# Kernel optimization log

Measured on AMD Instinct MI355X. Metric: run time of the kernel, lower is better.

Reference implementation:

```python
import jax, jax.numpy as jnp
import numpy as np

E, D, A, F, K = 512, 1024, 128, 32, 31  # encoder_dim, decoder_dim, attention_dim, location_filters, kernel
B, T = 128, 512


def setup_inputs() -> dict:
    key = jax.random.key(0)
    ks = jax.random.split(key, 9)
    s = lambda *sh: 1.0 / np.sqrt(sh[-1])
    return {
        "encoder_outputs": jax.random.normal(ks[0], (B, T, E), jnp.float32),
        "decoder_state": jax.random.normal(ks[1], (B, D), jnp.float32),
        "prev_attention_weights": jax.random.uniform(ks[2], (B, T), jnp.float32),
        # parameters (torch Linear stores [out, in]; Conv1d [out, in, K])
        "W_enc": jax.random.normal(ks[3], (A, E), jnp.float32) * s(A, E),
        "W_dec": jax.random.normal(ks[4], (A, D), jnp.float32) * s(A, D),
        "conv_w": jax.random.normal(ks[5], (F, 1, K), jnp.float32) * (1.0 / np.sqrt(K)),
        "W_loc": jax.random.normal(ks[6], (A, F), jnp.float32) * s(A, F),
        "W_e": jax.random.normal(ks[7], (1, A), jnp.float32) * s(1, A),
        "b_e": jax.random.normal(ks[8], (1,), jnp.float32) * 0.01,
    }


def reference(encoder_outputs, decoder_state, prev_attention_weights,
              W_enc, W_dec, conv_w, W_loc, W_e, b_e):
    # encoder projection: [B,T,E] @ [E,A] -> [B,T,A]
    enc_p = jnp.einsum('bte,ae->bta', encoder_outputs, W_enc)
    # decoder projection: [B,D] -> [B,1,A]
    dec_p = jnp.einsum('bd,ad->ba', decoder_state, W_dec)[:, None, :]
    # location conv: [B,1,T] * [F,1,K] -> [B,F,T], 'same' padding
    loc = jax.lax.conv_general_dilated(
        prev_attention_weights[:, None, :], conv_w,
        window_strides=(1,), padding=[((K - 1) // 2, (K - 1) // 2)],
        dimension_numbers=('NCH', 'OIH', 'NCH'))
    # [B,F,T] -> [B,T,A]
    loc_p = jnp.einsum('bft,af->bta', loc, W_loc)
    # energies: [B,T]
    energies = jnp.einsum('bta,a->bt', jnp.tanh(enc_p + dec_p + loc_p), W_e[0]) + b_e[0]
    attention_weights = jax.nn.softmax(energies, axis=1)
    # context: [B,T] x [B,T,E] -> [B,E]
    context_vector = jnp.einsum('bt,bte->be', attention_weights, encoder_outputs)
    return context_vector, attention_weights
```

## Files before the change

### kernel.cpp

```cpp
#include <hip/hip_runtime.h>
#include <hip/hip_bf16.h>
#include <math.h>

namespace {
constexpr int EDIM  = 512;
constexpr int DDIM  = 1024;
constexpr int ADIM  = 128;
constexpr int FDIM  = 32;
constexpr int KW    = 31;
constexpr int BATCH = 128;
constexpr int TDIM  = 512;

constexpr int LSTR = 40;
constexpr int TILE = 128 * LSTR;

typedef __attribute__((ext_vector_type(8))) short short8;
typedef __attribute__((ext_vector_type(4))) float floatx4;

__device__ __forceinline__ float fast_tanh(float x) {
  x = fminf(9.0f, fmaxf(-9.0f, x));
  float e = __expf(2.0f * x);
  return (e - 1.0f) / (e + 1.0f);
}

__device__ __forceinline__ ushort2 pack_bf16(float x, float y) {
  union { __hip_bfloat162 h; ushort2 u; } cv;
  cv.h = __float22bfloat162_rn(make_float2(x, y));
  return cv.u;
}

__device__ __forceinline__ short8 pack8(floatx4 a, floatx4 b) {
  union { ushort2 u[4]; short8 v; } o;
  o.u[0] = pack_bf16(a[0], a[1]); o.u[1] = pack_bf16(a[2], a[3]);
  o.u[2] = pack_bf16(b[0], b[1]); o.u[3] = pack_bf16(b[2], b[3]);
  return o.v;
}

__device__ __forceinline__ int ld_acq(int* p) {
  return __hip_atomic_load(p, __ATOMIC_ACQUIRE, __HIP_MEMORY_SCOPE_WORKGROUP);
}
__device__ __forceinline__ void add_rel(int* p) {
  __hip_atomic_fetch_add(p, 1, __ATOMIC_RELEASE, __HIP_MEMORY_SCOPE_WORKGROUP);
}

__global__ __launch_bounds__(256)
void dec_proj_kernel(const float* __restrict__ dec,
                     const float* __restrict__ Wdec,
                     float* __restrict__ dec_p) {
  int b = blockIdx.x, az = blockIdx.y;
  int tid = threadIdx.x;
  int al = tid >> 3, seg = tid & 7;
  int a = az * 32 + al;
  const float* dv = dec + (size_t)b * DDIM;
  const float* wv = Wdec + (size_t)a * DDIM;
  float s = 0.f;
  #pragma unroll 8
  for (int it = 0; it < 32; ++it) {
    int d = it * 32 + seg * 4;
    float4 d4 = *(const float4*)(dv + d);
    float4 w4 = *(const float4*)(wv + d);
    s += d4.x * w4.x + d4.y * w4.y + d4.z * w4.z + d4.w * w4.w;
  }
  s += __shfl_xor(s, 1, 64);
  s += __shfl_xor(s, 2, 64);
  s += __shfl_xor(s, 4, 64);
  if (seg == 0) dec_p[b * ADIM + a] = s;
}

template <int FUSED>
__global__ __launch_bounds__(768)
void energies_kernel(const float* __restrict__ enc,
                     const float* __restrict__ Wenc,
                     const float* __restrict__ pa,
                     const float* __restrict__ convw,
                     const float* __restrict__ Wloc,
                     const float* __restrict__ We,
                     const float* __restrict__ be,
                     const float* __restrict__ dec_p_g,
                     const float* __restrict__ dec,
                     const float* __restrict__ Wdec,
                     float* __restrict__ energ,
                     float* __restrict__ pm,
                     float* __restrict__ ps,
                     float* __restrict__ pctx) {
  __shared__ ushort tiles[2 * 2 * TILE];
  __shared__ ushort convS[4096];
  __shared__ float pa_s[160];
  __shared__ float cw_t[KW * 32];
  __shared__ int ready_a[2], ready_b[2], done_c[2], conv_done, dp_done;
  __shared__ float e_s[128];
  __shared__ float aw_s[128];
  __shared__ float ms[2];
  __shared__ float red2[6][512];
  __shared__ float dps[ADIM];

  const int tid  = threadIdx.x;
  const int b    = blockIdx.y;
  const int chunk = blockIdx.x;
  const int t0b  = chunk * 128;
  const int wave = tid >> 6, lane = tid & 63;

  if (tid == 0) {
    ready_a[0] = ready_a[1] = ready_b[0] = ready_b[1] = 0;
    done_c[0] = done_c[1] = 0;
    conv_done = 0;
    dp_done = 0;
  }
  if (tid >= 512 && tid < 512 + 158) {
    int gt = t0b - 15 + (tid - 512);
    pa_s[tid - 512] = (gt >= 0 && gt < TDIM) ? pa[b * TDIM + gt] : 0.f;
  }
  if (tid < 512)
    for (int id = tid; id < FDIM * KW; id += 512)
      cw_t[(id % KW) * 32 + (id / KW)] = convw[id];
  __syncthreads();

  if (wave >= 8) {
    const bool isA = (wave < 10);
    const int p = wave & 1;
    const float* gbase = isA ? enc + ((size_t)(b * TDIM + t0b)) * EDIM : Wenc;
    ushort* lbase = tiles + (isA ? 0 : TILE);
    int* myready = isA ? ready_a : ready_b;

    floatx4 v[8];
    #pragma unroll
    for (int j = 0; j < 4; ++j) {
      int idx = j * 64 + lane;
      int row = p * 64 + (idx >> 2), c = idx & 3;
      const float* g = gbase + (size_t)row * EDIM + c * 8;
      v[2 * j]     = *(const floatx4*)g;
      v[2 * j + 1] = *(const floatx4*)(g + 4);
    }

    for (int kt = 0; kt < 16; ++kt) {
      const int s = kt & 1, i = kt >> 1;
      if (kt >= 2)
        while (ld_acq(&done_c[s]) < 8 * i) __builtin_amdgcn_s_sleep(10);
      ushort* slot = lbase + s * 2 * TILE;
      #pragma unroll
      for (int j = 0; j < 4; ++j) {
        int idx = j * 64 + lane;
        int row = p * 64 + (idx >> 2), c = idx & 3;
        *(short8*)&slot[row * LSTR + c * 8] = pack8(v[2 * j], v[2 * j + 1]);
      }
      __threadfence_block();
      if (lane == 0) add_rel(&myready[s]);
      if (kt < 15) {
        #pragma unroll
        for (int j = 0; j < 4; ++j) {
          int idx = j * 64 + lane;
          int row = p * 64 + (idx >> 2), c = idx & 3;
          const float* g = gbase + (size_t)row * EDIM + (kt + 1) * 32 + c * 8;
          v[2 * j]     = *(const floatx4*)g;
          v[2 * j + 1] = *(const floatx4*)(g + 4);
        }
      }
    }

    if constexpr (!FUSED) return;

    {
      const int pidx = (wave - 8) * 64 + lane;
      const int a = pidx >> 1, half = pidx & 1;
      const float* dv = dec + (size_t)b * DDIM + half * 512;
      const float* wv = Wdec + (size_t)a * DDIM + half * 512;
      float s = 0.f;
      #pragma unroll 8
      for (int it = 0; it < 128; ++it) {
        floatx4 d4 = *(const floatx4*)(dv + it * 4);
        floatx4 w4 = *(const floatx4*)(wv + it * 4);
        s += d4[0] * w4[0] + d4[1] * w4[1] + d4[2] * w4[2] + d4[3] * w4[3];
      }
      s += __shfl_xor(s, 1, 64);
      if (half == 0) dps[a] = s;
      __threadfence_block();
      if (lane == 0) add_rel(&dp_done);
    }
  } else {
    const int lc = lane & 15, lq = lane >> 4;

    {
      const int tl = tid >> 2, fg = tid & 3;
      float cv[8] = {0.f, 0.f, 0.f, 0.f, 0.f, 0.f, 0.f, 0.f};
      #pragma unroll
      for (int k = 0; k < KW; ++k) {
        float p = pa_s[tl + k];
        floatx4 c0 = *(const floatx4*)&cw_t[k * 32 + fg * 8];
        floatx4 c1 = *(const floatx4*)&cw_t[k * 32 + fg * 8 + 4];
        #pragma unroll
        for (int n = 0; n < 4; ++n) cv[n] += p * c0[n];
        #pragma unroll
        for (int n = 0; n < 4; ++n) cv[4 + n] += p * c1[n];
      }
      *(short8*)&convS[tl * 32 + fg * 8] =
          pack8((floatx4){cv[0], cv[1], cv[2], cv[3]},
                (floatx4){cv[4], cv[5], cv[6], cv[7]});
    }
    __threadfence_block();
    if (lane == 0) add_rel(&conv_done);

    floatx4 acc[8];
    #pragma unroll
    for (int aT = 0; aT < 8; ++aT) acc[aT] = (floatx4){0.f, 0.f, 0.f, 0.f};

    for (int kt = 0; kt < 16; ++kt) {
      const int s = kt & 1, i = kt >> 1;
      const int need = 2 * (i + 1);
      while (ld_acq(&ready_a[s]) < need || ld_acq(&ready_b[s]) < need)
        __builtin_amdgcn_s_sleep(6);
      const ushort* As_ = tiles + s * 2 * TILE;
      const ushort* Bs_ = As_ + TILE;
      short8 af = *(const short8*)&As_[(wave * 16 + lc) * LSTR + lq * 8];
      #pragma unroll
      for (int aT = 0; aT < 8; ++aT) {
        short8 bf = *(const short8*)&Bs_[(aT * 16 + lc) * LSTR + lq * 8];
        acc[aT] = __builtin_amdgcn_mfma_f32_16x16x32_bf16(af, bf, acc[aT], 0, 0, 0);
      }
      if (lane == 0) add_rel(&done_c[s]);
    }

    while (ld_acq(&conv_done) < 8) __builtin_amdgcn_s_sleep(6);
    {
      short8 afl = *(const short8*)&convS[(wave * 16 + lc) * 32 + lq * 8];
      #pragma unroll
      for (int aT = 0; aT < 8; ++aT) {
        const float* g = Wloc + (size_t)(aT * 16 + lc) * FDIM + lq * 8;
        short8 bfl = pack8(*(const floatx4*)g, *(const floatx4*)(g + 4));
        acc[aT] = __builtin_amdgcn_mfma_f32_16x16x32_bf16(afl, bfl, acc[aT], 0, 0, 0);
      }
    }

    const float be0 = be[0];
    float dpv[8], wev[8];
    if constexpr (FUSED) {
      while (ld_acq(&dp_done) < 4) __builtin_amdgcn_s_sleep(6);
    }
    #pragma unroll
    for (int aT = 0; aT < 8; ++aT) {
      int a = aT * 16 + lc;
      dpv[aT] = FUSED ? dps[a] : dec_p_g[b * ADIM + a];
      wev[aT] = We[a];
    }
    {
      float es[4] = {0.f, 0.f, 0.f, 0.f};
      #pragma unroll
      for (int aT = 0; aT < 8; ++aT)
        #pragma unroll
        for (int i = 0; i < 4; ++i)
          es[i] += fast_tanh(acc[aT][i] + dpv[aT]) * wev[aT];
      #pragma unroll
      for (int m = 1; m < 16; m <<= 1)
        #pragma unroll
        for (int i = 0; i < 4; ++i) es[i] += __shfl_xor(es[i], m, 64);
      if (lc == 0) {
        floatx4 ev = {es[0] + be0, es[1] + be0, es[2] + be0, es[3] + be0};
        *(floatx4*)&energ[(size_t)b * TDIM + t0b + wave * 16 + lq * 4] = ev;
        if (FUSED) *(floatx4*)&e_s[wave * 16 + lq * 4] = ev;
      }
    }
  }

  if constexpr (!FUSED) return;

  __syncthreads();

  if (wave == 0) {
    float x0 = e_s[lane], x1 = e_s[lane + 64];
    float m = fmaxf(x0, x1);
    #pragma unroll
    for (int off = 1; off < 64; off <<= 1) m = fmaxf(m, __shfl_xor(m, off, 64));
    float sum = __expf(x0 - m) + __expf(x1 - m);
    #pragma unroll
    for (int off = 1; off < 64; off <<= 1) sum += __shfl_xor(sum, off, 64);
    if (lane == 0) {
      ms[0] = m;
      pm[b * 4 + chunk] = m;
      ps[b * 4 + chunk] = sum;
    }
  }
  __syncthreads();
  const float mI = ms[0];
  if (tid < 128) aw_s[tid] = __expf(e_s[tid] - mI);
  __syncthreads();

  {
    const int tg = tid >> 7;
    const int c4 = (tid & 127) * 4;
    const float* ep = enc + ((size_t)(b * TDIM + t0b)) * EDIM + c4;
    float4 acc = make_float4(0.f, 0.f, 0.f, 0.f);
    for (int t = tg; t < 128; t += 6) {
      float w = aw_s[t];
      float4 v = *(const float4*)(ep + (size_t)t * EDIM);
      acc.x += w * v.x; acc.y += w * v.y; acc.z += w * v.z; acc.w += w * v.w;
    }
    *(float4*)&red2[tg][c4] = acc;
  }
  __syncthreads();
  if (tid < 512) {
    float v = 0.f;
    #pragma unroll
    for (int g = 0; g < 6; ++g) v += red2[g][tid];
    pctx[((size_t)(b * 4 + chunk)) * EDIM + tid] = v;
  }
}

__global__ __launch_bounds__(512)
void combine_kernel(const float* __restrict__ energ,
                    const float* __restrict__ pm,
                    const float* __restrict__ ps,
                    const float* __restrict__ pctx,
                    float* __restrict__ attn,
                    float* __restrict__ ctx) {
  const int b = blockIdx.x, tid = threadIdx.x;
  const float m0 = pm[b * 4 + 0], m1 = pm[b * 4 + 1];
  const float m2 = pm[b * 4 + 2], m3 = pm[b * 4 + 3];
  const float M = fmaxf(fmaxf(m0, m1), fmaxf(m2, m3));
  const float r0 = __expf(m0 - M), r1 = __expf(m1 - M);
  const float r2 = __expf(m2 - M), r3 = __expf(m3 - M);
  const float S = ps[b * 4 + 0] * r0 + ps[b * 4 + 1] * r1 +
                  ps[b * 4 + 2] * r2 + ps[b * 4 + 3] * r3;
  const float inv = 1.0f / S;
  const float e = energ[(size_t)b * TDIM + tid];
  attn[(size_t)b * TDIM + tid] = __expf(e - M) * inv;
  const float* pc = pctx + (size_t)b * 4 * EDIM + tid;
  const float c = pc[0] * r0 + pc[EDIM] * r1 + pc[2 * EDIM] * r2 +
                  pc[3 * EDIM] * r3;
  ctx[(size_t)b * EDIM + tid] = c * inv;
}

__global__ __launch_bounds__(256)
void softmax_context_inplace_kernel(const float* __restrict__ enc,
                                    float* __restrict__ attn,
                                    float* __restrict__ ctx) {
  __shared__ float aw[TDIM];
  __shared__ float redm[4];
  __shared__ float reds[4];
  const int b = blockIdx.y, tid = threadIdx.x;
  float* row = attn + (size_t)b * TDIM;
  float x0 = row[tid], x1 = row[tid + 256];
  float m = fmaxf(x0, x1);
  #pragma unroll
  for (int off = 32; off; off >>= 1) m = fmaxf(m, __shfl_xor(m, off, 64));
  int wid = tid >> 6, lane = tid & 63;
  if (lane == 0) redm[wid] = m;
  __syncthreads();
  m = fmaxf(fmaxf(redm[0], redm[1]), fmaxf(redm[2], redm[3]));
  float e0 = __expf(x0 - m), e1 = __expf(x1 - m);
  float s = e0 + e1;
  #pragma unroll
  for (int off = 32; off; off >>= 1) s += __shfl_xor(s, off, 64);
  if (lane == 0) reds[wid] = s;
  __syncthreads();
  s = reds[0] + reds[1] + reds[2] + reds[3];
  float inv = 1.0f / s;
  float w0 = e0 * inv, w1 = e1 * inv;
  row[tid] = w0; row[tid + 256] = w1;
  aw[tid] = w0; aw[tid + 256] = w1;
  __syncthreads();
  const float* ep = enc + ((size_t)b * TDIM) * EDIM;
  float a0 = 0.f, a1 = 0.f;
  #pragma unroll 8
  for (int t = 0; t < TDIM; ++t) {
    float w = aw[t];
    a0 += w * ep[(size_t)t * EDIM + tid];
    a1 += w * ep[(size_t)t * EDIM + tid + 256];
  }
  ctx[(size_t)b * EDIM + tid] = a0;
  ctx[(size_t)b * EDIM + tid + 256] = a1;
}

}

extern "C" void kernel_launch(void* const* d_in, const int* in_sizes, int n_in,
                              void* d_out, int out_size, void* d_ws, size_t ws_size,
                              hipStream_t stream) {
  const float* enc   = (const float*)d_in[0];
  const float* dec   = (const float*)d_in[1];
  const float* pa    = (const float*)d_in[2];
  const float* Wenc  = (const float*)d_in[3];
  const float* Wdec  = (const float*)d_in[4];
  const float* convw = (const float*)d_in[5];
  const float* Wloc  = (const float*)d_in[6];
  const float* We    = (const float*)d_in[7];
  const float* be    = (const float*)d_in[8];

  float* ctx  = (float*)d_out;
  float* attn = (float*)d_out + BATCH * EDIM;

  float* energ = (float*)d_ws;
  float* pm    = energ + BATCH * TDIM;
  float* ps    = pm + BATCH * 4;
  float* pctx  = ps + BATCH * 4;

  const size_t need =
      ((size_t)BATCH * TDIM + BATCH * 8 + (size_t)BATCH * 4 * EDIM) *
      sizeof(float);

  dim3 g2(TDIM / 128, BATCH);
  if (ws_size >= need) {
    energies_kernel<1><<<g2, 768, 0, stream>>>(enc, Wenc, pa, convw, Wloc, We,
                                               be, nullptr, dec, Wdec,
                                               energ, pm, ps, pctx);
    combine_kernel<<<dim3(BATCH), 512, 0, stream>>>(energ, pm, ps, pctx,
                                                    attn, ctx);
  } else if (ws_size >= (size_t)BATCH * ADIM * sizeof(float)) {
    float* dec_p = (float*)d_ws;
    dim3 g1(BATCH, 4);
    dec_proj_kernel<<<g1, 256, 0, stream>>>(dec, Wdec, dec_p);
    energies_kernel<0><<<g2, 768, 0, stream>>>(enc, Wenc, pa, convw, Wloc, We,
                                               be, dec_p, nullptr, nullptr,
                                               attn, nullptr, nullptr, nullptr);
    dim3 g3(1, BATCH);
    softmax_context_inplace_kernel<<<g3, 256, 0, stream>>>(enc, attn, ctx);
  }
}
```

Before: 279.8 us.

## Keep full bf16 encoder tile resident in LDS and reuse it for context

The producer waves now write the whole 128x512 encoder chunk in bf16 into shared memory once, instead of double-buffering 32-wide slices. The context weighted sum then reads encoder values from LDS in bf16 rather than re-reading fp32 from global memory. The goal is to drop the second global read of the encoder tile. Other changes: the conv output reuses the B buffer after the GEMM, and the decoder projection is split across two waves instead of four. The cost is a much larger LDS footprint, which may lower occupancy, and lower context precision because it now accumulates from bf16 inputs.

Result: slower. 309.4 us (+10.6%).

```diff
diff --git a/kernel.cpp b/kernel.cpp
--- a/kernel.cpp
+++ b/kernel.cpp
@@ -11,8 +11,8 @@
 constexpr int BATCH = 128;
 constexpr int TDIM  = 512;
 
-constexpr int LSTR = 40;
-constexpr int TILE = 128 * LSTR;
+constexpr int ASTR = 520;
+constexpr int BSTR = 40;
 
 typedef __attribute__((ext_vector_type(8))) short short8;
 typedef __attribute__((ext_vector_type(4))) float floatx4;
@@ -41,6 +41,13 @@
 }
 __device__ __forceinline__ void add_rel(int* p) {
   __hip_atomic_fetch_add(p, 1, __ATOMIC_RELEASE, __HIP_MEMORY_SCOPE_WORKGROUP);
+}
+
+__device__ __forceinline__ float bf16_lo(unsigned v) {
+  union { unsigned u; float f; } c; c.u = v << 16; return c.f;
+}
+__device__ __forceinline__ float bf16_hi(unsigned v) {
+  union { unsigned u; float f; } c; c.u = v & 0xffff0000u; return c.f;
 }
 
 __global__ __launch_bounds__(256)
@@ -83,16 +90,15 @@
                      float* __restrict__ pm,
                      float* __restrict__ ps,
                      float* __restrict__ pctx) {
-  __shared__ ushort tiles[2 * 2 * TILE];
-  __shared__ ushort convS[4096];
+  __shared__ ushort A_s[128 * ASTR];
+  __shared__ ushort B_s[2 * 128 * BSTR];
+  __shared__ float cw_t[KW * 32];
   __shared__ float pa_s[160];
-  __shared__ float cw_t[KW * 32];
-  __shared__ int ready_a[2], ready_b[2], done_c[2], conv_done, dp_done;
   __shared__ float e_s[128];
-  __shared__ float aw_s[128];
-  __shared__ float ms[2];
-  __shared__ float red2[6][512];
   __shared__ float dps[ADIM];
+  __shared__ float2 red_c[256];
+  __shared__ float ms[1];
+  __shared__ int ready_a0, ready_a1, ready_b[2], done_b[2], conv_done, dp_done;
 
   const int tid  = threadIdx.x;
   const int b    = blockIdx.y;
@@ -101,8 +107,9 @@
   const int wave = tid >> 6, lane = tid & 63;
 
   if (tid == 0) {
-    ready_a[0] = ready_a[1] = ready_b[0] = ready_b[1] = 0;
-    done_c[0] = done_c[1] = 0;
+    ready_a0 = ready_a1 = 0;
+    ready_b[0] = ready_b[1] = 0;
+    done_b[0] = done_b[1] = 0;
     conv_done = 0;
     dp_done = 0;
   }
@@ -116,72 +123,96 @@
   __syncthreads();
 
   if (wave >= 8) {
-    const bool isA = (wave < 10);
     const int p = wave & 1;
-    const float* gbase = isA ? enc + ((size_t)(b * TDIM + t0b)) * EDIM : Wenc;
-    ushort* lbase = tiles + (isA ? 0 : TILE);
-    int* myready = isA ? ready_a : ready_b;
-
-    floatx4 v[8];
-    #pragma unroll
-    for (int j = 0; j < 4; ++j) {
-      int idx = j * 64 + lane;
-      int row = p * 64 + (idx >> 2), c = idx & 3;
-      const float* g = gbase + (size_t)row * EDIM + c * 8;
-      v[2 * j]     = *(const floatx4*)g;
-      v[2 * j + 1] = *(const floatx4*)(g + 4);
-    }
-
-    for (int kt = 0; kt < 16; ++kt) {
-      const int s = kt & 1, i = kt >> 1;
-      if (kt >= 2)
-        while (ld_acq(&done_c[s]) < 8 * i) __builtin_amdgcn_s_sleep(10);
-      ushort* slot = lbase + s * 2 * TILE;
+    if (wave < 10) {
+      int* myra = (p == 0) ? &ready_a0 : &ready_a1;
+      const float* gbase = enc + ((size_t)(b * TDIM + t0b)) * EDIM;
+      floatx4 v[8];
       #pragma unroll
       for (int j = 0; j < 4; ++j) {
         int idx = j * 64 + lane;
         int row = p * 64 + (idx >> 2), c = idx & 3;
-        *(short8*)&slot[row * LSTR + c * 8] = pack8(v[2 * j], v[2 * j + 1]);
-      }
-      __threadfence_block();
-      if (lane == 0) add_rel(&myready[s]);
-      if (kt < 15) {
+        const float* g = gbase + (size_t)row * EDIM + c * 8;
+        v[2 * j]     = *(const floatx4*)g;
+        v[2 * j + 1] = *(const floatx4*)(g + 4);
+      }
+      for (int kt = 0; kt < 16; ++kt) {
         #pragma unroll
         for (int j = 0; j < 4; ++j) {
           int idx = j * 64 + lane;
           int row = p * 64 + (idx >> 2), c = idx & 3;
-          const float* g = gbase + (size_t)row * EDIM + (kt + 1) * 32 + c * 8;
-          v[2 * j]     = *(const floatx4*)g;
-          v[2 * j + 1] = *(const floatx4*)(g + 4);
+          *(short8*)&A_s[row * ASTR + kt * 32 + c * 8] =
+              pack8(v[2 * j], v[2 * j + 1]);
         }
-      }
-    }
-
-    if constexpr (!FUSED) return;
-
-    {
-      const int pidx = (wave - 8) * 64 + lane;
-      const int a = pidx >> 1, half = pidx & 1;
-      const float* dv = dec + (size_t)b * DDIM + half * 512;
-      const float* wv = Wdec + (size_t)a * DDIM + half * 512;
-      float s = 0.f;
-      #pragma unroll 8
-      for (int it = 0; it < 128; ++it) {
-        floatx4 d4 = *(const floatx4*)(dv + it * 4);
-        floatx4 w4 = *(const floatx4*)(wv + it * 4);
-        s += d4[0] * w4[0] + d4[1] * w4[1] + d4[2] * w4[2] + d4[3] * w4[3];
-      }
-      s += __shfl_xor(s, 1, 64);
-      if (half == 0) dps[a] = s;
-      __threadfence_block();
-      if (lane == 0) add_rel(&dp_done);
+        __threadfence_block();
+        if (lane == 0) add_rel(myra);
+        if (kt < 15) {
+          #pragma unroll
+          for (int j = 0; j < 4; ++j) {
+            int idx = j * 64 + lane;
+            int row = p * 64 + (idx >> 2), c = idx & 3;
+            const float* g = gbase + (size_t)row * EDIM + (kt + 1) * 32 + c * 8;
+            v[2 * j]     = *(const floatx4*)g;
+            v[2 * j + 1] = *(const floatx4*)(g + 4);
+          }
+        }
+      }
+      if constexpr (FUSED) {
+        const int a = (wave - 8) * 64 + lane;
+        const float* dv = dec + (size_t)b * DDIM;
+        const float* wv = Wdec + (size_t)a * DDIM;
+        float s = 0.f;
+        #pragma unroll 8
+        for (int it = 0; it < 256; ++it) {
+          floatx4 d4 = *(const floatx4*)(dv + it * 4);
+          floatx4 w4 = *(const floatx4*)(wv + it * 4);
+          s += d4[0] * w4[0] + d4[1] * w4[1] + d4[2] * w4[2] + d4[3] * w4[3];
+        }
+        dps[a] = s;
+        __threadfence_block();
+        if (lane == 0) add_rel(&dp_done);
+      }
+    } else {
+      floatx4 v[8];
+      #pragma unroll
+      for (int j = 0; j < 4; ++j) {
+        int idx = j * 64 + lane;
+        int row = p * 64 + (idx >> 2), c = idx & 3;
+        const float* g = Wenc + (size_t)row * EDIM + c * 8;
+        v[2 * j]     = *(const floatx4*)g;
+        v[2 * j + 1] = *(const floatx4*)(g + 4);
+      }
+      for (int kt = 0; kt < 16; ++kt) {
+        const int s = kt & 1, i = kt >> 1;
+        if (kt >= 2)
+          while (ld_acq(&done_b[s]) < 8 * i) __builtin_amdgcn_s_sleep(10);
+        ushort* slot = B_s + s * 128 * BSTR;
+        #pragma unroll
+        for (int j = 0; j < 4; ++j) {
+          int idx = j * 64 + lane;
+          int row = p * 64 + (idx >> 2), c = idx & 3;
+          *(short8*)&slot[row * BSTR + c * 8] = pack8(v[2 * j], v[2 * j + 1]);
+        }
+        __threadfence_block();
+        if (lane == 0) add_rel(&ready_b[s]);
+        if (kt < 15) {
+          #pragma unroll
+          for (int j = 0; j < 4; ++j) {
+            int idx = j * 64 + lane;
+            int row = p * 64 + (idx >> 2), c = idx & 3;
+            const float* g = Wenc + (size_t)row * EDIM + (kt + 1) * 32 + c * 8;
+            v[2 * j]     = *(const floatx4*)g;
+            v[2 * j + 1] = *(const floatx4*)(g + 4);
+          }
+        }
+      }
     }
   } else {
     const int lc = lane & 15, lq = lane >> 4;
 
+    float cv[8] = {0.f, 0.f, 0.f, 0.f, 0.f, 0.f, 0.f, 0.f};
     {
       const int tl = tid >> 2, fg = tid & 3;
-      float cv[8] = {0.f, 0.f, 0.f, 0.f, 0.f, 0.f, 0.f, 0.f};
       #pragma unroll
       for (int k = 0; k < KW; ++k) {
         float p = pa_s[tl + k];
@@ -192,12 +223,7 @@
         #pragma unroll
         for (int n = 0; n < 4; ++n) cv[4 + n] += p * c1[n];
       }
-      *(short8*)&convS[tl * 32 + fg * 8] =
-          pack8((floatx4){cv[0], cv[1], cv[2], cv[3]},
-                (floatx4){cv[4], cv[5], cv[6], cv[7]});
-    }
-    __threadfence_block();
-    if (lane == 0) add_rel(&conv_done);
+    }
 
     floatx4 acc[8];
     #pragma unroll
@@ -205,23 +231,32 @@
 
     for (int kt = 0; kt < 16; ++kt) {
       const int s = kt & 1, i = kt >> 1;
-      const int need = 2 * (i + 1);
-      while (ld_acq(&ready_a[s]) < need || ld_acq(&ready_b[s]) < need)
+      const int need_a = kt + 1, need_b = 2 * (i + 1);
+      while (ld_acq(&ready_a0) < need_a || ld_acq(&ready_a1) < need_a ||
+             ld_acq(&ready_b[s]) < need_b)
         __builtin_amdgcn_s_sleep(6);
-      const ushort* As_ = tiles + s * 2 * TILE;
-      const ushort* Bs_ = As_ + TILE;
-      short8 af = *(const short8*)&As_[(wave * 16 + lc) * LSTR + lq * 8];
+      short8 af = *(const short8*)&A_s[(wave * 16 + lc) * ASTR + kt * 32 + lq * 8];
+      const ushort* Bs_ = B_s + s * 128 * BSTR;
       #pragma unroll
       for (int aT = 0; aT < 8; ++aT) {
-        short8 bf = *(const short8*)&Bs_[(aT * 16 + lc) * LSTR + lq * 8];
+        short8 bf = *(const short8*)&Bs_[(aT * 16 + lc) * BSTR + lq * 8];
         acc[aT] = __builtin_amdgcn_mfma_f32_16x16x32_bf16(af, bf, acc[aT], 0, 0, 0);
       }
-      if (lane == 0) add_rel(&done_c[s]);
-    }
-
+      if (lane == 0) add_rel(&done_b[s]);
+    }
+
+    while (ld_acq(&done_b[0]) < 64) __builtin_amdgcn_s_sleep(6);
+    {
+      const int row = wave * 16 + (lane >> 2), fg = lane & 3;
+      *(short8*)&B_s[row * BSTR + fg * 8] =
+          pack8((floatx4){cv[0], cv[1], cv[2], cv[3]},
+                (floatx4){cv[4], cv[5], cv[6], cv[7]});
+    }
+    __threadfence_block();
+    if (lane == 0) add_rel(&conv_done);
     while (ld_acq(&conv_done) < 8) __builtin_amdgcn_s_sleep(6);
     {
-      short8 afl = *(const short8*)&convS[(wave * 16 + lc) * 32 + lq * 8];
+      short8 afl = *(const short8*)&B_s[(wave * 16 + lc) * BSTR + lq * 8];
       #pragma unroll
       for (int aT = 0; aT < 8; ++aT) {
         const float* g = Wloc + (size_t)(aT * 16 + lc) * FDIM + lq * 8;
@@ -233,7 +268,7 @@
     const float be0 = be[0];
     float dpv[8], wev[8];
     if constexpr (FUSED) {
-      while (ld_acq(&dp_done) < 4) __builtin_amdgcn_s_sleep(6);
+      while (ld_acq(&dp_done) < 2) __builtin_amdgcn_s_sleep(6);
     }
     #pragma unroll
     for (int aT = 0; aT < 8; ++aT) {
@@ -280,27 +315,26 @@
   }
   __syncthreads();
   const float mI = ms[0];
-  if (tid < 128) aw_s[tid] = __expf(e_s[tid] - mI);
-  __syncthreads();
-
-  {
-    const int tg = tid >> 7;
-    const int c4 = (tid & 127) * 4;
-    const float* ep = enc + ((size_t)(b * TDIM + t0b)) * EDIM + c4;
-    float4 acc = make_float4(0.f, 0.f, 0.f, 0.f);
-    for (int t = tg; t < 128; t += 6) {
-      float w = aw_s[t];
-      float4 v = *(const float4*)(ep + (size_t)t * EDIM);
-      acc.x += w * v.x; acc.y += w * v.y; acc.z += w * v.z; acc.w += w * v.w;
-    }
-    *(float4*)&red2[tg][c4] = acc;
-  }
-  __syncthreads();
+  if (tid < 128) e_s[tid] = __expf(e_s[tid] - mI);
+  __syncthreads();
+
+  float2 cacc = make_float2(0.f, 0.f);
+  const int g = tid >> 8, cp = tid & 255;
   if (tid < 512) {
-    float v = 0.f;
-    #pragma unroll
-    for (int g = 0; g < 6; ++g) v += red2[g][tid];
-    pctx[((size_t)(b * 4 + chunk)) * EDIM + tid] = v;
+    #pragma unroll 8
+    for (int t = g * 64; t < g * 64 + 64; ++t) {
+      float w = e_s[t];
+      unsigned v = *(const unsigned*)&A_s[t * ASTR + 2 * cp];
+      cacc.x += w * bf16_lo(v);
+      cacc.y += w * bf16_hi(v);
+    }
+    if (g == 1) red_c[cp] = cacc;
+  }
+  __syncthreads();
+  if (tid < 256) {
+    float2 o = red_c[cp];
+    o.x += cacc.x; o.y += cacc.y;
+    *(float2*)&pctx[((size_t)(b * 4 + chunk)) * EDIM + 2 * cp] = o;
   }
 }
 
```
